# Kernel tuning notes

Measured on AMD Instinct MI355X. Metric: run time of the kernel, lower is better.

## Reference

```python
import jax, jax.numpy as jnp
import numpy as np

N_ITER = 10
EPS = 1e-20
REG = 1e-6


def _nmf(Tn, Vn, Yn):
    # Tn [I,K], Vn [K,J], Yn [I,J] complex. T,V are strictly positive, so
    # torch's .abs() on Rn is the identity.
    Rn = Tn @ Vn
    Y_d_R = jnp.abs(Yn) ** 2 / (Rn ** 2 + EPS)
    Rn_d = 1.0 / (Rn + EPS)
    Tn = Tn * jnp.sqrt((Y_d_R @ Vn.T) / (Rn_d @ Vn.T + EPS))
    Vn = Vn * jnp.sqrt((Tn.T @ Y_d_R) / (Tn.T @ Rn_d + EPS))
    Rn_new = Tn @ Vn
    return Tn, Vn, Rn_new


def _forward(X, T0, V0):
    M, J, I, _ = X.shape
    N = M
    # [M,J,I,2] real -> [I,M,J] complex64
    X_c = (X[..., 0] + 1j * X[..., 1]).astype(jnp.complex64).transpose(2, 0, 1)
    eye = jnp.eye(M, dtype=jnp.complex64)
    W = jnp.broadcast_to(eye[None], (I, M, M)).astype(jnp.complex64) + jnp.zeros((I, M, M), jnp.complex64)
    Y = jnp.einsum('inm,imj->inj', W, X_c)  # [I,N,J]
    T = T0
    V = V0

    def body(carry, _):
        W, Y, T, V = carry
        for n in range(N):  # N == 2, structurally small static loop
            Tn, Vn, Rn = _nmf(T[:, :, n], V[:, :, n], Y[:, n, :])
            T = T.at[:, :, n].set(Tn)
            V = V.at[:, :, n].set(Vn)
            inv_sqrt_Rn = jnp.sqrt(1.0 / (Rn + EPS))  # [I,J] real
            Xw = X_c * inv_sqrt_Rn[:, None, :]  # [I,M,J] complex
            D = Xw @ jnp.conj(Xw).transpose(0, 2, 1) / J + REG * eye[None]  # [I,M,M]
            A = W @ D
            e_n = jnp.broadcast_to(eye[:, n][None, :, None], (D.shape[0], M, 1))
            b = jnp.linalg.solve(A, e_n)  # [I,M,1]
            bH = jnp.conj(b).transpose(0, 2, 1)
            denom = jnp.sqrt((bH @ D @ b).real + EPS)  # [I,1,1]
            w = jnp.conj((b / denom)[:, :, 0])  # [I,M]
            W = W.at[:, n, :].set(w)
        Y = jnp.einsum('inm,imj->inj', W, X_c)
        return (W, Y, T, V), None

    (W, Y, T, V), _ = jax.lax.scan(body, (W, Y, T, V), None, length=N_ITER)
    Y_out = Y.transpose(1, 2, 0)  # [N,J,I]
    return jnp.stack([Y_out.real, Y_out.imag], axis=-1)  # [N,J,I,2]


def setup_inputs() -> dict:
    key = jax.random.key(0)
    k1, k2, k3 = jax.random.split(key, 3)
    M, J, I, K = 2, 1024, 1025, 8
    X = jax.random.normal(k1, (M, J, I, 2), dtype=jnp.float32)
    T0 = jax.random.uniform(k2, (I, K, M), dtype=jnp.float32) * (1 - 1e-8) + 1e-8
    V0 = jax.random.uniform(k3, (K, J, M), dtype=jnp.float32) * (1 - 1e-8) + 1e-8
    return {"X": X, "T0": T0, "V0": V0}


def reference(X, T0, V0):
    return _forward(X, T0, V0)
```

## Files before the change

### kernel.cpp

```cpp
#include <hip/hip_runtime.h>
#include <math.h>

#define I_DIM 1025
#define J_DIM 1024
#define K_DIM 8
#define N_ITER 10
#define EPS 1e-20f
#define REG 1e-6f
#define MODE_CD  1
#define MODE_NMF 2

__device__ __forceinline__ float2 cmul(float2 a, float2 b){
  return make_float2(a.x*b.x - a.y*b.y, a.x*b.y + a.y*b.x);
}
__device__ __forceinline__ float2 cadd(float2 a, float2 b){
  return make_float2(a.x+b.x, a.y+b.y);
}
__device__ __forceinline__ float2 csub(float2 a, float2 b){
  return make_float2(a.x-b.x, a.y-b.y);
}
__device__ __forceinline__ float2 cconj(float2 a){ return make_float2(a.x, -a.y); }
__device__ __forceinline__ float2 cscale(float2 a, float s){ return make_float2(a.x*s, a.y*s); }
__device__ __forceinline__ float2 cdivc(float2 a, float2 d){
  float inv = 1.0f/(d.x*d.x + d.y*d.y);
  return make_float2((a.x*d.x + a.y*d.y)*inv, (a.y*d.x - a.x*d.y)*inv);
}

__global__ void k_init(const float* __restrict__ T0, const float* __restrict__ V0,
                       float* __restrict__ Tw, float* __restrict__ Vw, float2* __restrict__ Wm){
  int tid = blockIdx.x*blockDim.x + threadIdx.x;
  if (tid < 2*I_DIM*K_DIM){
    int n = tid/(I_DIM*K_DIM), rem = tid%(I_DIM*K_DIM);
    int i = rem/K_DIM, k = rem%K_DIM;
    Tw[tid] = T0[(i*K_DIM+k)*2 + n];
  }
  if (tid < 2*K_DIM*J_DIM){
    int n = tid/(K_DIM*J_DIM), rem = tid%(K_DIM*J_DIM);
    int k = rem/J_DIM, j = rem%J_DIM;
    Vw[tid] = V0[(k*J_DIM+j)*2 + n];
  }
  if (tid < I_DIM*4){
    int rc = tid & 3;
    Wm[tid] = make_float2((rc==0||rc==3)?1.0f:0.0f, 0.0f);
  }
}

__global__ void k_txpose(const float2* __restrict__ Xin, float4* __restrict__ Xc4){
  __shared__ float4 tile[32][33];
  int i0 = blockIdx.x*32, j0 = blockIdx.y*32;
  int tx = threadIdx.x, ty = threadIdx.y;
  #pragma unroll
  for (int r=0;r<4;r++){
    int jl = ty + r*8; int i = i0 + tx;
    if (i < I_DIM){
      float2 a = Xin[(size_t)(0*J_DIM + j0 + jl)*I_DIM + i];
      float2 b = Xin[(size_t)(1*J_DIM + j0 + jl)*I_DIM + i];
      tile[jl][tx] = make_float4(a.x, a.y, b.x, b.y);
    }
  }
  __syncthreads();
  #pragma unroll
  for (int r=0;r<4;r++){
    int il = ty + r*8; int i = i0 + il;
    if (i < I_DIM) Xc4[(size_t)i*J_DIM + j0 + tx] = tile[tx][il];
  }
}

__global__ __launch_bounds__(256) void k_cda(const float4* __restrict__ Xc4,
      float* __restrict__ Tw, float* __restrict__ Told, const float* __restrict__ Vw,
      float2* __restrict__ Wm, int mode){
  int i = blockIdx.x, tid = threadIdx.x;
  int n = tid >> 7, jl = tid & 127;
  __shared__ float redD[4][4];
  __shared__ float redT[4][16];
  __shared__ float wsh[8];

  float t[8];
  {
    const float4* tp = (const float4*)&Tw[(size_t)(n*I_DIM+i)*K_DIM];
    float4 ta = tp[0], tb = tp[1];
    t[0]=ta.x; t[1]=ta.y; t[2]=ta.z; t[3]=ta.w;
    t[4]=tb.x; t[5]=tb.y; t[6]=tb.z; t[7]=tb.w;
  }
  float r_s[8] = {0,0,0,0,0,0,0,0};
  #pragma unroll
  for (int k=0;k<8;k++){
    const float4* vp = (const float4*)&Vw[(size_t)(n*K_DIM+k)*J_DIM + jl*8];
    float4 va = vp[0], vb = vp[1];
    r_s[0]+=t[k]*va.x; r_s[1]+=t[k]*va.y; r_s[2]+=t[k]*va.z; r_s[3]+=t[k]*va.w;
    r_s[4]+=t[k]*vb.x; r_s[5]+=t[k]*vb.y; r_s[6]+=t[k]*vb.z; r_s[7]+=t[k]*vb.w;
  }
  float4 x_s[8];
  #pragma unroll
  for (int s=0;s<8;s++) x_s[s] = Xc4[(size_t)i*J_DIM + jl*8 + s];

  if (mode & MODE_CD){
    float d00=0.0f, d11=0.0f, dre=0.0f, dim_=0.0f;
    #pragma unroll
    for (int s=0;s<8;s++){
      float4 x = x_s[s];
      float q = 1.0f/(r_s[s] + EPS);
      d00 += (x.x*x.x + x.y*x.y)*q;
      d11 += (x.z*x.z + x.w*x.w)*q;
      dre += (x.x*x.z + x.y*x.w)*q;
      dim_ += (x.y*x.z - x.x*x.w)*q;
    }
    #pragma unroll
    for (int off=32; off>0; off>>=1){
      d00 += __shfl_down(d00,off); d11 += __shfl_down(d11,off);
      dre += __shfl_down(dre,off); dim_ += __shfl_down(dim_,off);
    }
    {
      int lane = tid&63, wv = tid>>6;
      if (lane==0){ redD[wv][0]=d00; redD[wv][1]=d11; redD[wv][2]=dre; redD[wv][3]=dim_; }
    }
    __syncthreads();
    if (tid==0){
      const float invJ = 1.0f/(float)J_DIM;
      float D[2][4];
      #pragma unroll
      for (int c=0;c<4;c++){
        D[0][c] = (redD[0][c]+redD[1][c])*invJ;
        D[1][c] = (redD[2][c]+redD[3][c])*invJ;
      }
      float2 w00 = Wm[i*4+0], w01 = Wm[i*4+1], w10 = Wm[i*4+2], w11 = Wm[i*4+3];
      #pragma unroll
      for (int nn=0;nn<2;nn++){
        float d00_ = D[nn][0] + REG, d11_ = D[nn][1] + REG;
        float2 d01 = make_float2(D[nn][2], D[nn][3]);
        float2 d10 = cconj(d01);
        float2 A00 = cadd(cscale(w00, d00_), cmul(w01, d10));
        float2 A01 = cadd(cmul(w00, d01), cscale(w01, d11_));
        float2 A10 = cadd(cscale(w10, d00_), cmul(w11, d10));
        float2 A11 = cadd(cmul(w10, d01), cscale(w11, d11_));
        float2 det = csub(cmul(A00,A11), cmul(A01,A10));
        float2 bu0, bu1;
        if (nn==0){ bu0 = A11; bu1 = make_float2(-A10.x, -A10.y); }
        else      { bu0 = make_float2(-A01.x, -A01.y); bu1 = A00; }
        float2 b0 = cdivc(bu0, det);
        float2 b1 = cdivc(bu1, det);
        float quad = d00_*(b0.x*b0.x + b0.y*b0.y) + d11_*(b1.x*b1.x + b1.y*b1.y);
        float2 u = cmul(d01, b1);
        quad += 2.0f*(b0.x*u.x + b0.y*u.y);
        float inv = 1.0f/sqrtf(quad + EPS);
        float2 wn0 = make_float2(b0.x*inv, -b0.y*inv);
        float2 wn1 = make_float2(b1.x*inv, -b1.y*inv);
        if (nn==0){ w00=wn0; w01=wn1; } else { w10=wn0; w11=wn1; }
      }
      Wm[i*4+0]=w00; Wm[i*4+1]=w01; Wm[i*4+2]=w10; Wm[i*4+3]=w11;
      wsh[0]=w00.x; wsh[1]=w00.y; wsh[2]=w01.x; wsh[3]=w01.y;
      wsh[4]=w10.x; wsh[5]=w10.y; wsh[6]=w11.x; wsh[7]=w11.y;
    }
  } else {
    if (tid < 4){ float2 w = Wm[i*4+tid]; wsh[tid*2]=w.x; wsh[tid*2+1]=w.y; }
  }
  __syncthreads();
  if (!(mode & MODE_NMF)) return;

  if ((tid & 127) < 8){
    int kk = tid & 7;
    Told[(size_t)(n*I_DIM+i)*K_DIM + kk] = t[kk];
  }

  float2 w0 = make_float2(wsh[n*4+0], wsh[n*4+1]);
  float2 w1 = make_float2(wsh[n*4+2], wsh[n*4+3]);
  float p_s[8], q_s[8];
  #pragma unroll
  for (int s=0;s<8;s++){
    float4 x = x_s[s];
    float yre = w0.x*x.x - w0.y*x.y + w1.x*x.z - w1.y*x.w;
    float yim = w0.x*x.y + w0.y*x.x + w1.x*x.w + w1.y*x.z;
    float y2 = yre*yre + yim*yim;
    float r = r_s[s];
    p_s[s] = y2/(r*r + EPS);
    q_s[s] = 1.0f/(r + EPS);
  }
  float aN[8], aD[8];
  #pragma unroll
  for (int k=0;k<8;k++){
    const float4* vp = (const float4*)&Vw[(size_t)(n*K_DIM+k)*J_DIM + jl*8];
    float4 va = vp[0], vb = vp[1];
    aN[k] = p_s[0]*va.x + p_s[1]*va.y + p_s[2]*va.z + p_s[3]*va.w
          + p_s[4]*vb.x + p_s[5]*vb.y + p_s[6]*vb.z + p_s[7]*vb.w;
    aD[k] = q_s[0]*va.x + q_s[1]*va.y + q_s[2]*va.z + q_s[3]*va.w
          + q_s[4]*vb.x + q_s[5]*vb.y + q_s[6]*vb.z + q_s[7]*vb.w;
  }
  #pragma unroll
  for (int k=0;k<8;k++){
    #pragma unroll
    for (int off=32; off>0; off>>=1){
      aN[k] += __shfl_down(aN[k],off);
      aD[k] += __shfl_down(aD[k],off);
    }
  }
  {
    int lane = tid&63, wv = tid>>6;
    if (lane==0){
      #pragma unroll
      for (int k=0;k<8;k++){ redT[wv][k]=aN[k]; redT[wv][k+8]=aD[k]; }
    }
  }
  __syncthreads();
  if ((tid & 127) < 8){
    int kk = tid & 7;
    int wb = (tid>>7)*2;
    float ns = redT[wb][kk]   + redT[wb+1][kk];
    float ds = redT[wb][kk+8] + redT[wb+1][kk+8];
    size_t ti = (size_t)(n*I_DIM+i)*K_DIM + kk;
    Tw[ti] = Tw[ti]*sqrtf(ns/(ds + EPS));
  }
}

__global__ __launch_bounds__(256) void k_vupd(const float4* __restrict__ Xc4,
      const float* __restrict__ Tw, const float* __restrict__ Told,
      float* __restrict__ Vw, const float2* __restrict__ Wm){
  int n = blockIdx.y;
  int tid = threadIdx.x;
  int jj = tid & 3, ii = tid >> 2;
  int j = blockIdx.x*4 + jj;
  float v[8];
  #pragma unroll
  for (int k=0;k<8;k++) v[k] = Vw[(size_t)(n*K_DIM+k)*J_DIM + j];
  float aN[8] = {0,0,0,0,0,0,0,0};
  float aD[8] = {0,0,0,0,0,0,0,0};
  for (int i=ii; i<I_DIM; i+=64){
    const float4* tpo = (const float4*)&Told[(size_t)(n*I_DIM+i)*K_DIM];
    float4 to0 = tpo[0], to1 = tpo[1];
    const float4* tpn = (const float4*)&Tw[(size_t)(n*I_DIM+i)*K_DIM];
    float4 tn0 = tpn[0], tn1 = tpn[1];
    float4 wv = *(const float4*)&Wm[i*4 + n*2];
    float4 x  = Xc4[(size_t)i*J_DIM + j];
    float r = to0.x*v[0]+to0.y*v[1]+to0.z*v[2]+to0.w*v[3]
            + to1.x*v[4]+to1.y*v[5]+to1.z*v[6]+to1.w*v[7];
    float yre = wv.x*x.x - wv.y*x.y + wv.z*x.z - wv.w*x.w;
    float yim = wv.x*x.y + wv.y*x.x + wv.z*x.w + wv.w*x.z;
    float y2 = yre*yre + yim*yim;
    float p = y2/(r*r + EPS);
    float q = 1.0f/(r + EPS);
    aN[0]+=tn0.x*p; aN[1]+=tn0.y*p; aN[2]+=tn0.z*p; aN[3]+=tn0.w*p;
    aN[4]+=tn1.x*p; aN[5]+=tn1.y*p; aN[6]+=tn1.z*p; aN[7]+=tn1.w*p;
    aD[0]+=tn0.x*q; aD[1]+=tn0.y*q; aD[2]+=tn0.z*q; aD[3]+=tn0.w*q;
    aD[4]+=tn1.x*q; aD[5]+=tn1.y*q; aD[6]+=tn1.z*q; aD[7]+=tn1.w*q;
  }
  #pragma unroll
  for (int k=0;k<8;k++){
    #pragma unroll
    for (int off=32; off>=4; off>>=1){
      aN[k] += __shfl_down(aN[k],off);
      aD[k] += __shfl_down(aD[k],off);
    }
  }
  __shared__ float red[4][4][16];
  int wv_ = tid>>6, lane = tid&63;
  if (lane < 4){
    #pragma unroll
    for (int k=0;k<8;k++){ red[wv_][lane][k]=aN[k]; red[wv_][lane][k+8]=aD[k]; }
  }
  __syncthreads();
  if (tid < 32){
    int jj2 = tid>>3, k = tid&7;
    float num = red[0][jj2][k]+red[1][jj2][k]+red[2][jj2][k]+red[3][jj2][k];
    float den = red[0][jj2][k+8]+red[1][jj2][k+8]+red[2][jj2][k+8]+red[3][jj2][k+8];
    size_t vi = (size_t)(n*K_DIM+k)*J_DIM + blockIdx.x*4 + jj2;
    Vw[vi] *= sqrtf(num/(den + EPS));
  }
}

__global__ void k_final(const float4* __restrict__ Xc4, const float2* __restrict__ Wm,
                        float2* __restrict__ out){
  __shared__ float2 yt[2][32][33];
  int i0 = blockIdx.x*32, j0 = blockIdx.y*32;
  int tx = threadIdx.x, ty = threadIdx.y;
  int j = j0 + tx;
  #pragma unroll
  for (int r=0;r<4;r++){
    int il = ty + r*8; int i = i0 + il;
    if (i < I_DIM){
      float4 x = Xc4[(size_t)i*J_DIM + j];
      #pragma unroll
      for (int n=0;n<2;n++){
        float2 a = Wm[i*4+n*2+0], b = Wm[i*4+n*2+1];
        float2 y;
        y.x = a.x*x.x - a.y*x.y + b.x*x.z - b.y*x.w;
        y.y = a.x*x.y + a.y*x.x + b.x*x.w + b.y*x.z;
        yt[n][tx][il] = y;
      }
    }
  }
  __syncthreads();
  int i = i0 + tx;
  if (i < I_DIM){
    #pragma unroll
    for (int n=0;n<2;n++){
      #pragma unroll
      for (int r=0;r<4;r++){
        int jl = ty + r*8;
        out[(size_t)(n*J_DIM + j0 + jl)*I_DIM + i] = yt[n][jl][tx];
      }
    }
  }
}

extern "C" void kernel_launch(void* const* d_in, const int* in_sizes, int n_in,
                              void* d_out, int out_size, void* d_ws, size_t ws_size,
                              hipStream_t stream){
  const float* X  = (const float*)d_in[0];
  const float* T0 = (const float*)d_in[1];
  const float* V0 = (const float*)d_in[2];

  char* ws = (char*)d_ws;
  size_t off = 0;
  auto alloc = [&](size_t bytes)->char*{
    char* p = ws + off; off += (bytes + 255) & ~(size_t)255; return p;
  };
  float4* Xc4  = (float4*)alloc((size_t)I_DIM*J_DIM*sizeof(float4));
  float*  Tw   = (float*) alloc((size_t)2*I_DIM*K_DIM*sizeof(float));
  float*  Told = (float*) alloc((size_t)2*I_DIM*K_DIM*sizeof(float));
  float*  Vw   = (float*) alloc((size_t)2*K_DIM*J_DIM*sizeof(float));
  float2* Wm   = (float2*)alloc((size_t)I_DIM*4*sizeof(float2));

  k_init<<<65, 256, 0, stream>>>(T0, V0, Tw, Vw, Wm);
  k_txpose<<<dim3(33,32), dim3(32,8), 0, stream>>>((const float2*)X, Xc4);
  k_cda<<<I_DIM, 256, 0, stream>>>(Xc4, Tw, Told, Vw, Wm, MODE_NMF);
  for (int it=0; it<N_ITER; it++){
    k_vupd<<<dim3(J_DIM/4, 2), 256, 0, stream>>>(Xc4, Tw, Told, Vw, Wm);
    int mode = (it < N_ITER-1) ? (MODE_CD|MODE_NMF) : MODE_CD;
    k_cda<<<I_DIM, 256, 0, stream>>>(Xc4, Tw, Told, Vw, Wm, mode);
  }
  k_final<<<dim3(33,32), dim3(32,8), 0, stream>>>(Xc4, Wm, (float2*)d_out);
}
```

Baseline: 331.9 us.

## Transpose T to K-major layout, coalesce J strides, use fast reciprocals

Stores T (and Told) in K-major [n][k][i] layout so k_vupd threads with consecutive i read contiguous addresses. k_cda switches from each thread owning eight consecutive j to a 128-strided assignment, so X and V loads coalesce across lanes. Divisions are replaced by hardware reciprocal approximations, and the reciprocal of R is reused for both the D accumulation and the NMF terms. The approximate reciprocal may slightly change numerics, and per-thread vector loads become scalar loads.

Measured after the change: 311.7 us. 1.06x faster.

```diff
diff --git a/kernel.cpp b/kernel.cpp
--- a/kernel.cpp
+++ b/kernel.cpp
@@ -10,6 +10,8 @@
 #define MODE_CD  1
 #define MODE_NMF 2
 
+__device__ __forceinline__ float __frcp(float x){ return __builtin_amdgcn_rcpf(x); }
+
 __device__ __forceinline__ float2 cmul(float2 a, float2 b){
   return make_float2(a.x*b.x - a.y*b.y, a.x*b.y + a.y*b.x);
 }
@@ -29,9 +31,9 @@
 __global__ void k_init(const float* __restrict__ T0, const float* __restrict__ V0,
                        float* __restrict__ Tw, float* __restrict__ Vw, float2* __restrict__ Wm){
   int tid = blockIdx.x*blockDim.x + threadIdx.x;
-  if (tid < 2*I_DIM*K_DIM){
-    int n = tid/(I_DIM*K_DIM), rem = tid%(I_DIM*K_DIM);
-    int i = rem/K_DIM, k = rem%K_DIM;
+  if (tid < 2*K_DIM*I_DIM){
+    int i = tid % I_DIM; int rest = tid / I_DIM;
+    int k = rest & 7, n = rest >> 3;
     Tw[tid] = T0[(i*K_DIM+k)*2 + n];
   }
   if (tid < 2*K_DIM*J_DIM){
@@ -76,30 +78,30 @@
   __shared__ float wsh[8];
 
   float t[8];
-  {
-    const float4* tp = (const float4*)&Tw[(size_t)(n*I_DIM+i)*K_DIM];
-    float4 ta = tp[0], tb = tp[1];
-    t[0]=ta.x; t[1]=ta.y; t[2]=ta.z; t[3]=ta.w;
-    t[4]=tb.x; t[5]=tb.y; t[6]=tb.z; t[7]=tb.w;
-  }
+  #pragma unroll
+  for (int k=0;k<8;k++) t[k] = Tw[(size_t)(n*K_DIM+k)*I_DIM + i];
+
+  const float* vb = Vw + (size_t)(n*K_DIM)*J_DIM + jl;
   float r_s[8] = {0,0,0,0,0,0,0,0};
   #pragma unroll
   for (int k=0;k<8;k++){
-    const float4* vp = (const float4*)&Vw[(size_t)(n*K_DIM+k)*J_DIM + jl*8];
-    float4 va = vp[0], vb = vp[1];
-    r_s[0]+=t[k]*va.x; r_s[1]+=t[k]*va.y; r_s[2]+=t[k]*va.z; r_s[3]+=t[k]*va.w;
-    r_s[4]+=t[k]*vb.x; r_s[5]+=t[k]*vb.y; r_s[6]+=t[k]*vb.z; r_s[7]+=t[k]*vb.w;
-  }
+    #pragma unroll
+    for (int s=0;s<8;s++) r_s[s] += t[k]*vb[k*J_DIM + 128*s];
+  }
+  float q_s[8];
+  #pragma unroll
+  for (int s=0;s<8;s++) q_s[s] = __frcp(r_s[s] + EPS);
+
+  const float4* xb = Xc4 + (size_t)i*J_DIM + jl;
   float4 x_s[8];
   #pragma unroll
-  for (int s=0;s<8;s++) x_s[s] = Xc4[(size_t)i*J_DIM + jl*8 + s];
+  for (int s=0;s<8;s++) x_s[s] = xb[128*s];
 
   if (mode & MODE_CD){
     float d00=0.0f, d11=0.0f, dre=0.0f, dim_=0.0f;
     #pragma unroll
     for (int s=0;s<8;s++){
-      float4 x = x_s[s];
-      float q = 1.0f/(r_s[s] + EPS);
+      float4 x = x_s[s]; float q = q_s[s];
       d00 += (x.x*x.x + x.y*x.y)*q;
       d11 += (x.z*x.z + x.w*x.w)*q;
       dre += (x.x*x.z + x.y*x.w)*q;
@@ -159,31 +161,30 @@
 
   if ((tid & 127) < 8){
     int kk = tid & 7;
-    Told[(size_t)(n*I_DIM+i)*K_DIM + kk] = t[kk];
+    Told[(size_t)(n*K_DIM+kk)*I_DIM + i] = t[kk];
   }
 
   float2 w0 = make_float2(wsh[n*4+0], wsh[n*4+1]);
   float2 w1 = make_float2(wsh[n*4+2], wsh[n*4+3]);
-  float p_s[8], q_s[8];
+  float p_s[8];
   #pragma unroll
   for (int s=0;s<8;s++){
     float4 x = x_s[s];
     float yre = w0.x*x.x - w0.y*x.y + w1.x*x.z - w1.y*x.w;
     float yim = w0.x*x.y + w0.y*x.x + w1.x*x.w + w1.y*x.z;
-    float y2 = yre*yre + yim*yim;
-    float r = r_s[s];
-    p_s[s] = y2/(r*r + EPS);
-    q_s[s] = 1.0f/(r + EPS);
+    float q = q_s[s];
+    p_s[s] = (yre*yre + yim*yim)*q*q;
   }
   float aN[8], aD[8];
   #pragma unroll
   for (int k=0;k<8;k++){
-    const float4* vp = (const float4*)&Vw[(size_t)(n*K_DIM+k)*J_DIM + jl*8];
-    float4 va = vp[0], vb = vp[1];
-    aN[k] = p_s[0]*va.x + p_s[1]*va.y + p_s[2]*va.z + p_s[3]*va.w
-          + p_s[4]*vb.x + p_s[5]*vb.y + p_s[6]*vb.z + p_s[7]*vb.w;
-    aD[k] = q_s[0]*va.x + q_s[1]*va.y + q_s[2]*va.z + q_s[3]*va.w
-          + q_s[4]*vb.x + q_s[5]*vb.y + q_s[6]*vb.z + q_s[7]*vb.w;
+    float sn = 0.0f, sd = 0.0f;
+    #pragma unroll
+    for (int s=0;s<8;s++){
+      float v = vb[k*J_DIM + 128*s];
+      sn += p_s[s]*v; sd += q_s[s]*v;
+    }
+    aN[k] = sn; aD[k] = sd;
   }
   #pragma unroll
   for (int k=0;k<8;k++){
@@ -206,8 +207,8 @@
     int wb = (tid>>7)*2;
     float ns = redT[wb][kk]   + redT[wb+1][kk];
     float ds = redT[wb][kk+8] + redT[wb+1][kk+8];
-    size_t ti = (size_t)(n*I_DIM+i)*K_DIM + kk;
-    Tw[ti] = Tw[ti]*sqrtf(ns/(ds + EPS));
+    size_t ti = (size_t)(n*K_DIM+kk)*I_DIM + i;
+    Tw[ti] = Tw[ti]*sqrtf(ns*__frcp(ds + EPS));
   }
 }
 
@@ -223,24 +224,23 @@
   for (int k=0;k<8;k++) v[k] = Vw[(size_t)(n*K_DIM+k)*J_DIM + j];
   float aN[8] = {0,0,0,0,0,0,0,0};
   float aD[8] = {0,0,0,0,0,0,0,0};
+  const float* tob = Told + (size_t)(n*K_DIM)*I_DIM;
+  const float* tnb = Tw   + (size_t)(n*K_DIM)*I_DIM;
+  #pragma unroll 2
   for (int i=ii; i<I_DIM; i+=64){
-    const float4* tpo = (const float4*)&Told[(size_t)(n*I_DIM+i)*K_DIM];
-    float4 to0 = tpo[0], to1 = tpo[1];
-    const float4* tpn = (const float4*)&Tw[(size_t)(n*I_DIM+i)*K_DIM];
-    float4 tn0 = tpn[0], tn1 = tpn[1];
+    float to[8], tn[8];
+    #pragma unroll
+    for (int k=0;k<8;k++){ to[k] = tob[k*I_DIM + i]; tn[k] = tnb[k*I_DIM + i]; }
     float4 wv = *(const float4*)&Wm[i*4 + n*2];
     float4 x  = Xc4[(size_t)i*J_DIM + j];
-    float r = to0.x*v[0]+to0.y*v[1]+to0.z*v[2]+to0.w*v[3]
-            + to1.x*v[4]+to1.y*v[5]+to1.z*v[6]+to1.w*v[7];
+    float r = to[0]*v[0]+to[1]*v[1]+to[2]*v[2]+to[3]*v[3]
+            + to[4]*v[4]+to[5]*v[5]+to[6]*v[6]+to[7]*v[7];
     float yre = wv.x*x.x - wv.y*x.y + wv.z*x.z - wv.w*x.w;
     float yim = wv.x*x.y + wv.y*x.x + wv.z*x.w + wv.w*x.z;
-    float y2 = yre*yre + yim*yim;
-    float p = y2/(r*r + EPS);
-    float q = 1.0f/(r + EPS);
-    aN[0]+=tn0.x*p; aN[1]+=tn0.y*p; aN[2]+=tn0.z*p; aN[3]+=tn0.w*p;
-    aN[4]+=tn1.x*p; aN[5]+=tn1.y*p; aN[6]+=tn1.z*p; aN[7]+=tn1.w*p;
-    aD[0]+=tn0.x*q; aD[1]+=tn0.y*q; aD[2]+=tn0.z*q; aD[3]+=tn0.w*q;
-    aD[4]+=tn1.x*q; aD[5]+=tn1.y*q; aD[6]+=tn1.z*q; aD[7]+=tn1.w*q;
+    float q = __frcp(r + EPS);
+    float p = (yre*yre + yim*yim)*q*q;
+    #pragma unroll
+    for (int k=0;k<8;k++){ aN[k] += tn[k]*p; aD[k] += tn[k]*q; }
   }
   #pragma unroll
   for (int k=0;k<8;k++){
@@ -262,7 +262,7 @@
     float num = red[0][jj2][k]+red[1][jj2][k]+red[2][jj2][k]+red[3][jj2][k];
     float den = red[0][jj2][k+8]+red[1][jj2][k+8]+red[2][jj2][k+8]+red[3][jj2][k+8];
     size_t vi = (size_t)(n*K_DIM+k)*J_DIM + blockIdx.x*4 + jj2;
-    Vw[vi] *= sqrtf(num/(den + EPS));
+    Vw[vi] *= sqrtf(num*__frcp(den + EPS));
   }
 }
 
@@ -314,8 +314,8 @@
     char* p = ws + off; off += (bytes + 255) & ~(size_t)255; return p;
   };
   float4* Xc4  = (float4*)alloc((size_t)I_DIM*J_DIM*sizeof(float4));
-  float*  Tw   = (float*) alloc((size_t)2*I_DIM*K_DIM*sizeof(float));
-  float*  Told = (float*) alloc((size_t)2*I_DIM*K_DIM*sizeof(float));
+  float*  Tw   = (float*) alloc((size_t)2*K_DIM*I_DIM*sizeof(float));
+  float*  Told = (float*) alloc((size_t)2*K_DIM*I_DIM*sizeof(float));
   float*  Vw   = (float*) alloc((size_t)2*K_DIM*J_DIM*sizeof(float));
   float2* Wm   = (float2*)alloc((size_t)I_DIM*4*sizeof(float2));
 
```
